# Kernel optimization log

Measured on AMD Instinct MI355X. Metric: run time of the kernel, lower is better.

## Reference

```python
import jax, jax.numpy as jnp
import numpy as np

EMBED_DIM = 768
NUM_HEADS = 12
HEAD_DIM = EMBED_DIM // NUM_HEADS
SCALING = HEAD_DIM ** -0.5


def setup_inputs() -> dict:
    key = jax.random.key(0)
    ks = jax.random.split(key, 12)
    B, S, E, H = 4, 1024, EMBED_DIM, NUM_HEADS
    inp = {
        "hidden_states": jax.random.normal(ks[0], (B, S, E), dtype=jnp.float32),
        "pos_row": jax.random.randint(ks[1], (B, S), 0, 64, dtype=jnp.int32),
        "pos_col": jax.random.randint(ks[2], (B, S), 0, 32, dtype=jnp.int32),
        "q_w": jax.random.normal(ks[3], (E, E), dtype=jnp.float32) * 0.02,
        "q_b": jnp.zeros((E,), dtype=jnp.float32),
        "k_w": jax.random.normal(ks[4], (E, E), dtype=jnp.float32) * 0.02,
        "k_b": jnp.zeros((E,), dtype=jnp.float32),
        "v_w": jax.random.normal(ks[5], (E, E), dtype=jnp.float32) * 0.02,
        "v_b": jnp.zeros((E,), dtype=jnp.float32),
        "o_w": jax.random.normal(ks[6], (E, E), dtype=jnp.float32) * 0.02,
        "o_b": jnp.zeros((E,), dtype=jnp.float32),
        "rel_table": jax.random.normal(ks[7], (4, H), dtype=jnp.float32) * 0.02,
    }
    return inp


def _generate_bias(pos_row, pos_col, rel_table):
    # relative row/col differences: [B, S, S]
    rel_row = pos_row[:, :, None] - pos_row[:, None, :]
    rel_col = pos_col[:, :, None] - pos_col[:, None, :]
    rel_cell = jnp.abs(rel_row) + jnp.abs(rel_col)
    # table index: other=0, same row=1, same col=2, same cell=3 (priority order as in torch code)
    idx = jnp.where(rel_row == 0, 1, 0)
    idx = jnp.where(rel_col == 0, 2, idx)
    idx = jnp.where(rel_cell == 0, 3, idx)
    # gather: [B, S, S, H] -> [B, H, S, S]
    bias = rel_table[idx]
    return jnp.transpose(bias, (0, 3, 1, 2))


def reference(hidden_states, pos_row, pos_col, q_w, q_b, k_w, k_b, v_w, v_b, o_w, o_b, rel_table):
    B, S, E = hidden_states.shape
    H, D = NUM_HEADS, HEAD_DIM

    def shape(x):  # [B, S, E] -> [B, H, S, D]
        return jnp.transpose(x.reshape(B, S, H, D), (0, 2, 1, 3))

    q = shape((hidden_states @ q_w.T + q_b) * SCALING)
    k = shape(hidden_states @ k_w.T + k_b)
    v = shape(hidden_states @ v_w.T + v_b)

    # [B, H, S, S]
    attn = jnp.einsum("bhqd,bhkd->bhqk", q, k)
    attn = attn + _generate_bias(pos_row, pos_col, rel_table)
    attn = jax.nn.softmax(attn, axis=-1)

    out = jnp.einsum("bhqk,bhkd->bhqd", attn, v)  # [B, H, S, D]
    out = jnp.transpose(out, (0, 2, 1, 3)).reshape(B, S, E)
    return out @ o_w.T + o_b
```

## Files before the change

kernel.cpp:

```cpp
#include <hip/hip_runtime.h>

#define NHEADS 12
#define HDIM   64
#define EMB    768
#define SEQ    1024
#define BATCH  4
#define MTOT   (BATCH * SEQ)

typedef __bf16 bf16x8 __attribute__((ext_vector_type(8)));
typedef float  f32x4  __attribute__((ext_vector_type(4)));

#define GLB(p) ((const __attribute__((address_space(1))) uint32_t*)(p))
#define LDS(p) ((__attribute__((address_space(3))) uint32_t*)(p))

__device__ __forceinline__ uint bfr(float f) {
    uint u = __float_as_uint(f);
    return (u + 0x7fffu + ((u >> 16) & 1u)) >> 16;
}

__global__ __launch_bounds__(256) void split_f32(
    const float* __restrict__ x, ushort* __restrict__ hi,
    ushort* __restrict__ lo, int n4)
{
    int i = blockIdx.x * 256 + threadIdx.x;
    if (i >= n4) return;
    float4 v = ((const float4*)x)[i];
    float f[4] = {v.x, v.y, v.z, v.w};
    ushort hh[4], ll[4];
#pragma unroll
    for (int j = 0; j < 4; ++j) {
        uint h = bfr(f[j]);
        float hf = __uint_as_float(h << 16);
        ll[j] = (ushort)bfr(f[j] - hf);
        hh[j] = (ushort)h;
    }
    ushort4 hv = {hh[0], hh[1], hh[2], hh[3]};
    ushort4 lv = {ll[0], ll[1], ll[2], ll[3]};
    ((ushort4*)hi)[i] = hv;
    ((ushort4*)lo)[i] = lv;
}

__global__ __launch_bounds__(256) void split_w4(
    const float* __restrict__ w0, const float* __restrict__ w1,
    const float* __restrict__ w2, const float* __restrict__ w3,
    ushort* __restrict__ wch, ushort* __restrict__ wcl,
    ushort* __restrict__ woh, ushort* __restrict__ wol, int n4)
{
    const int y = blockIdx.y;
    const float* src = (y == 0) ? w0 : (y == 1) ? w1 : (y == 2) ? w2 : w3;
    ushort* hi = (y < 3) ? (wch + (size_t)y * (EMB * EMB)) : woh;
    ushort* lo = (y < 3) ? (wcl + (size_t)y * (EMB * EMB)) : wol;
    int i = blockIdx.x * 256 + threadIdx.x;
    if (i >= n4) return;
    float4 v = ((const float4*)src)[i];
    float f[4] = {v.x, v.y, v.z, v.w};
    ushort hh[4], ll[4];
#pragma unroll
    for (int j = 0; j < 4; ++j) {
        uint h = bfr(f[j]);
        float hf = __uint_as_float(h << 16);
        ll[j] = (ushort)bfr(f[j] - hf);
        hh[j] = (ushort)h;
    }
    ushort4 hv = {hh[0], hh[1], hh[2], hh[3]};
    ushort4 lv = {ll[0], ll[1], ll[2], ll[3]};
    ((ushort4*)hi)[i] = hv;
    ((ushort4*)lo)[i] = lv;
}

template <int MODE, int BM>
__global__ __launch_bounds__(256) void gemm_mfma(
    const ushort* __restrict__ Ah, const ushort* __restrict__ Al,
    const ushort* __restrict__ Wh, const ushort* __restrict__ Wl,
    const float* __restrict__ b0, const float* __restrict__ b1,
    const float* __restrict__ b2,
    ushort* __restrict__ q16, ushort* __restrict__ k16,
    ushort* __restrict__ vT16, float* __restrict__ o0)
{
    constexpr int SA = BM * 64;
    constexpr int SB = 8192;
    constexpr int TS = 2 * SA + 2 * SB;
    constexpr int MFRAG = BM / 32;
    constexpr int WMS = BM / 2;

    __shared__ __align__(16) char ldsc[2 * TS];

    const int t  = threadIdx.x;
    const int w  = t >> 6;
    const int l  = t & 63;
    const int m0 = blockIdx.x * BM;
    const int n0 = blockIdx.y * 128;
    const int wm = w >> 1;
    const int wn = w & 1;

    const char* gb[4] = {
        (const char*)Ah + (size_t)m0 * 1536,
        (const char*)Al + (size_t)m0 * 1536,
        (const char*)Wh + (size_t)n0 * 1536,
        (const char*)Wl + (size_t)n0 * 1536};

    int aoff[MFRAG], boff[4];
#pragma unroll
    for (int i = 0; i < MFRAG; ++i) {
        int row = wm * WMS + i * 16 + (l & 15);
        aoff[i] = row * 64 + ((((l >> 4) ^ ((row >> 1) & 3))) << 4);
    }
#pragma unroll
    for (int i = 0; i < 4; ++i) {
        int rn = wn * 64 + i * 16 + (l & 15);
        boff[i] = rn * 64 + ((((l >> 4) ^ ((rn >> 1) & 3))) << 4);
    }

    auto stage = [&](int ks, int buf) {
        const size_t kb = (size_t)ks * 64;
        char* dst = ldsc + buf * TS;
#pragma unroll
        for (int tt = 0; tt < 4; ++tt) {
            const int tsz  = (tt < 2) ? SA : SB;
            const int tbas = (tt == 0) ? 0 : (tt == 1) ? SA : (tt == 2) ? 2 * SA : 2 * SA + SB;
#pragma unroll
            for (int p = 0; p < tsz; p += 4096) {
                const int soff = p + w * 1024 + l * 16;
                const int srow = soff >> 6;
                const int slot = (soff >> 4) & 3;
                const size_t go = (size_t)srow * 1536 +
                                  ((slot ^ ((srow >> 1) & 3)) << 4) + kb;
                __builtin_amdgcn_global_load_lds(GLB(gb[tt] + go),
                                                 LDS(dst + tbas + p + w * 1024), 16, 0, 0);
            }
        }
    };

    f32x4 acc[MFRAG][4] = {};

    stage(0, 0);
    __syncthreads();

    for (int ks = 0; ks < 24; ++ks) {
        if (ks + 1 < 24) stage(ks + 1, (ks + 1) & 1);

        const char* cur = ldsc + (ks & 1) * TS;
        bf16x8 ah[MFRAG], al[MFRAG], bh[4], bl[4];
#pragma unroll
        for (int i = 0; i < MFRAG; ++i) {
            ah[i] = *(const bf16x8*)(cur + aoff[i]);
            al[i] = *(const bf16x8*)(cur + SA + aoff[i]);
        }
#pragma unroll
        for (int i = 0; i < 4; ++i) {
            bh[i] = *(const bf16x8*)(cur + 2 * SA + boff[i]);
            bl[i] = *(const bf16x8*)(cur + 2 * SA + SB + boff[i]);
        }
#pragma unroll
        for (int i = 0; i < MFRAG; ++i)
#pragma unroll
            for (int j = 0; j < 4; ++j) {
                acc[i][j] = __builtin_amdgcn_mfma_f32_16x16x32_bf16(ah[i], bh[j], acc[i][j], 0, 0, 0);
                acc[i][j] = __builtin_amdgcn_mfma_f32_16x16x32_bf16(ah[i], bl[j], acc[i][j], 0, 0, 0);
                acc[i][j] = __builtin_amdgcn_mfma_f32_16x16x32_bf16(al[i], bh[j], acc[i][j], 0, 0, 0);
            }
        __syncthreads();
    }

    const int mrow_base = m0 + wm * WMS + ((l >> 4) << 2);

    if (MODE == 1) {
        const int which = (n0 >= 1536) ? 2 : (n0 >= 768 ? 1 : 0);
        const float* bp = (which == 0) ? b0 : (which == 1 ? b1 : b2);
        ushort* op = (which == 0) ? q16 : (which == 1 ? k16 : vT16);
        const float scale = (which == 0) ? 0.125f : 1.0f;
        const int nin_base = n0 - which * 768 + wn * 64 + (l & 15);
#pragma unroll
        for (int j = 0; j < 4; ++j) {
            const int n_in = nin_base + j * 16;
            const float bv = bp[n_in];
            const int h = n_in >> 6, d = n_in & 63;
#pragma unroll
            for (int i = 0; i < MFRAG; ++i)
#pragma unroll
                for (int r = 0; r < 4; ++r) {
                    const int m = mrow_base + i * 16 + r;
                    const int bb = m >> 10, s = m & 1023;
                    const ushort u = (ushort)bfr((acc[i][j][r] + bv) * scale);
                    const size_t dst = (which == 2)
                        ? ((size_t)((bb * NHEADS + h) * HDIM + d) * SEQ + s)
                        : ((size_t)((bb * NHEADS + h) * SEQ + s) * HDIM + d);
                    op[dst] = u;
                }
        }
    } else {
        const int nin_base = n0 + wn * 64 + (l & 15);
#pragma unroll
        for (int j = 0; j < 4; ++j) {
            const int n_in = nin_base + j * 16;
            const float bv = b0[n_in];
#pragma unroll
            for (int i = 0; i < MFRAG; ++i)
#pragma unroll
                for (int r = 0; r < 4; ++r) {
                    const int m = mrow_base + i * 16 + r;
                    o0[(size_t)m * 768 + n_in] = acc[i][j][r] + bv;
                }
        }
    }
}

#define QPOFF  0
#define KOFF   8192
#define VOFF   24576
#define POSOFF 40960

__global__ __launch_bounds__(256) void attn_mfma(
    const ushort* __restrict__ q16, const ushort* __restrict__ k16,
    const ushort* __restrict__ vT16, const int* __restrict__ pos_row,
    const int* __restrict__ pos_col, const float* __restrict__ rel_table,
    ushort* __restrict__ aoh, ushort* __restrict__ aol)
{
    __shared__ __align__(16) char lds[41472];

    const int t  = threadIdx.x;
    const int w  = t >> 6;
    const int l  = t & 63;
    const int bh = blockIdx.y;
    const int b  = bh / NHEADS;
    const int h  = bh - b * NHEADS;
    const int q0g = blockIdx.x * 64;

    const char* qb  = (const char*)(q16 + (size_t)bh * SEQ * HDIM);
    const char* kb  = (const char*)(k16 + (size_t)bh * SEQ * HDIM);
    const char* vtb = (const char*)(vT16 + (size_t)bh * HDIM * SEQ);

    const float t0 = rel_table[0 * NHEADS + h];
    const float t1 = rel_table[1 * NHEADS + h];
    const float t2 = rel_table[2 * NHEADS + h];
    const float t3 = rel_table[3 * NHEADS + h];

    const int o1 = t * 16, o2 = o1 + 4096;
    const int r1 = o1 >> 7, r2 = o2 >> 7;
    const int kq1 = o1 ^ ((r1 & 7) << 4);
    const int kq2 = o2 ^ ((r2 & 7) << 4);
    const int vs1 = r1 * 2048 + (((((o1 >> 4) & 7) ^ (r1 & 7))) << 4);
    const int vs2 = r2 * 2048 + (((((o2 >> 4) & 7) ^ (r2 & 7))) << 4);

    auto stage_kv = [&](int kt, int buf) {
        const int k0g = kt * 64;
        __builtin_amdgcn_global_load_lds(GLB(kb + (size_t)k0g * 128 + kq1),
                                         LDS(lds + KOFF + buf * 8192 + w * 1024), 16, 0, 0);
        __builtin_amdgcn_global_load_lds(GLB(kb + (size_t)k0g * 128 + kq2),
                                         LDS(lds + KOFF + buf * 8192 + w * 1024 + 4096), 16, 0, 0);
        __builtin_amdgcn_global_load_lds(GLB(vtb + (size_t)k0g * 2 + vs1),
                                         LDS(lds + VOFF + buf * 8192 + w * 1024), 16, 0, 0);
        __builtin_amdgcn_global_load_lds(GLB(vtb + (size_t)k0g * 2 + vs2),
                                         LDS(lds + VOFF + buf * 8192 + w * 1024 + 4096), 16, 0, 0);
        if (t < 64) {
            int pr = pos_row[b * SEQ + k0g + t];
            int pc = pos_col[b * SEQ + k0g + t];
            *(int*)(lds + POSOFF + buf * 256 + t * 4) = (pr << 8) | pc;
        }
    };

    __builtin_amdgcn_global_load_lds(GLB(qb + (size_t)q0g * 128 + kq1),
                                     LDS(lds + QPOFF + w * 1024), 16, 0, 0);
    __builtin_amdgcn_global_load_lds(GLB(qb + (size_t)q0g * 128 + kq2),
                                     LDS(lds + QPOFF + w * 1024 + 4096), 16, 0, 0);
    stage_kv(0, 0);

    const int qrow_g = q0g + w * 16 + (l & 15);
    const int pq = (pos_row[b * SEQ + qrow_g] << 8) | pos_col[b * SEQ + qrow_g];

    __syncthreads();

    bf16x8 qf[2];
    const int qrl = w * 16 + (l & 15);
#pragma unroll
    for (int ks = 0; ks < 2; ++ks)
        qf[ks] = *(const bf16x8*)(lds + QPOFF + qrl * 128 +
                                  ((((l >> 4) + 4 * ks) ^ (qrl & 7)) << 4));

    f32x4 pv[4] = {};
    float m_run = -1e30f, l_run = 0.0f;

    const int prow = l & 15;
    const int pswz = (prow & 7) << 4;
    const int pwbase = QPOFF + w * 2048 + prow * 128;

    for (int kt = 0; kt < 16; ++kt) {
        const int cb = kt & 1;
        if (kt + 1 < 16) stage_kv(kt + 1, cb ^ 1);
        const char* kbuf = lds + KOFF + cb * 8192;
        const char* vbuf = lds + VOFF + cb * 8192;
        const char* pbuf = lds + POSOFF + cb * 256;

        f32x4 sacc[4] = {};
#pragma unroll
        for (int ks = 0; ks < 2; ++ks) {
            const bf16x8 qq = qf[ks];
#pragma unroll
            for (int j = 0; j < 4; ++j) {
                const int krow = j * 16 + (l & 15);
                const bf16x8 kf = *(const bf16x8*)(kbuf + krow * 128 +
                                                   ((((l >> 4) + 4 * ks) ^ (krow & 7)) << 4));
                sacc[j] = __builtin_amdgcn_mfma_f32_16x16x32_bf16(kf, qq, sacc[j], 0, 0, 0);
            }
        }

        int4 pk4[4];
#pragma unroll
        for (int j = 0; j < 4; ++j)
            pk4[j] = *(const int4*)(pbuf + (l >> 4) * 16 + j * 64);

        float sv[16];
#pragma unroll
        for (int j = 0; j < 4; ++j) {
            const int pkk[4] = {pk4[j].x, pk4[j].y, pk4[j].z, pk4[j].w};
#pragma unroll
            for (int r = 0; r < 4; ++r) {
                const int dd = pq ^ pkk[r];
                const float bs = ((dd & 0xFF00) == 0)
                                     ? (((dd & 0xFF) == 0) ? t3 : t1)
                                     : (((dd & 0xFF) == 0) ? t2 : t0);
                sv[j * 4 + r] = sacc[j][r] + bs;
            }
        }
        float pm = sv[0];
#pragma unroll
        for (int i = 1; i < 16; ++i) pm = fmaxf(pm, sv[i]);
        pm = fmaxf(pm, __shfl_xor(pm, 16));
        pm = fmaxf(pm, __shfl_xor(pm, 32));
        const float mnew = fmaxf(m_run, pm);
        float psum = 0.0f;
#pragma unroll
        for (int i = 0; i < 16; ++i) {
            sv[i] = __expf(sv[i] - mnew);
            psum += sv[i];
        }
        psum += __shfl_xor(psum, 16);
        psum += __shfl_xor(psum, 32);
        const float alpha = __expf(m_run - mnew);
        l_run = l_run * alpha + psum;
        m_run = mnew;

#pragma unroll
        for (int r = 0; r < 4; ++r) {
            const float ar = __shfl(alpha, (l >> 4) * 4 + r);
#pragma unroll
            for (int i = 0; i < 4; ++i) pv[i][r] *= ar;
        }

#pragma unroll
        for (int j = 0; j < 4; ++j)
#pragma unroll
            for (int p2 = 0; p2 < 2; ++p2) {
                const uint u = bfr(sv[j * 4 + 2 * p2]) | (bfr(sv[j * 4 + 2 * p2 + 1]) << 16);
                const int adr = pwbase + (((l >> 4) * 8 + 4 * p2 + 32 * j) ^ pswz);
                *(uint*)(lds + adr) = u;
            }

#pragma unroll
        for (int ks = 0; ks < 2; ++ks) {
            const bf16x8 pf = *(const bf16x8*)(lds + pwbase +
                                               ((((l >> 4) + 4 * ks) << 4) ^ pswz));
#pragma unroll
            for (int i = 0; i < 4; ++i) {
                const int vrow = i * 16 + (l & 15);
                const bf16x8 vf = *(const bf16x8*)(vbuf + vrow * 128 +
                                                   ((((l >> 4) + 4 * ks) ^ (vrow & 7)) << 4));
                pv[i] = __builtin_amdgcn_mfma_f32_16x16x32_bf16(pf, vf, pv[i], 0, 0, 0);
            }
        }
        __syncthreads();
    }

    const float rinv = 1.0f / l_run;
#pragma unroll
    for (int r = 0; r < 4; ++r) {
        const float inv = __shfl(rinv, (l >> 4) * 4 + r);
        const int mrow = b * SEQ + q0g + w * 16 + (l >> 4) * 4 + r;
        const size_t base = (size_t)mrow * 768 + h * 64 + prow;
#pragma unroll
        for (int i = 0; i < 4; ++i) {
            const float o = pv[i][r] * inv;
            const uint hu = bfr(o);
            const float hf = __uint_as_float(hu << 16);
            const uint lu = bfr(o - hf);
            aoh[base + 16 * i] = (ushort)hu;
            aol[base + 16 * i] = (ushort)lu;
        }
    }
}

extern "C" void kernel_launch(void* const* d_in, const int* in_sizes, int n_in,
                              void* d_out, int out_size, void* d_ws, size_t ws_size,
                              hipStream_t stream)
{
    const float* hs      = (const float*)d_in[0];
    const int*   pos_row = (const int*)d_in[1];
    const int*   pos_col = (const int*)d_in[2];
    const float* q_w     = (const float*)d_in[3];
    const float* q_b     = (const float*)d_in[4];
    const float* k_w     = (const float*)d_in[5];
    const float* k_b     = (const float*)d_in[6];
    const float* v_w     = (const float*)d_in[7];
    const float* v_b     = (const float*)d_in[8];
    const float* o_w     = (const float*)d_in[9];
    const float* o_b     = (const float*)d_in[10];
    const float* rel_tab = (const float*)d_in[11];

    char* ws = (char*)d_ws;
    const size_t HS_N = (size_t)MTOT * EMB;
    const size_t W_N  = (size_t)EMB * EMB;
    ushort* hsh = (ushort*)ws;  ws += HS_N * 2;
    ushort* hsl = (ushort*)ws;  ws += HS_N * 2;
    ushort* wch = (ushort*)ws;  ws += 3 * W_N * 2;
    ushort* wcl = (ushort*)ws;  ws += 3 * W_N * 2;
    ushort* woh = (ushort*)ws;  ws += W_N * 2;
    ushort* wol = (ushort*)ws;  ws += W_N * 2;
    ushort* aoh = (ushort*)ws;  ws += HS_N * 2;
    ushort* aol = (ushort*)ws;  ws += HS_N * 2;
    ushort* q16 = (ushort*)ws;  ws += HS_N * 2;
    ushort* k16 = (ushort*)ws;  ws += HS_N * 2;
    ushort* vT16 = (ushort*)ws; ws += HS_N * 2;

    split_f32<<<(int)(HS_N / 4 / 256), 256, 0, stream>>>(hs, hsh, hsl, (int)(HS_N / 4));
    split_w4<<<dim3((int)(W_N / 4 / 256), 4), 256, 0, stream>>>(
        q_w, k_w, v_w, o_w, wch, wcl, woh, wol, (int)(W_N / 4));

    gemm_mfma<1, 128><<<dim3(MTOT / 128, 2304 / 128), 256, 0, stream>>>(
        hsh, hsl, wch, wcl, q_b, k_b, v_b, q16, k16, vT16, nullptr);

    attn_mfma<<<dim3(SEQ / 64, BATCH * NHEADS), 256, 0, stream>>>(
        q16, k16, vT16, pos_row, pos_col, rel_tab, aoh, aol);

    gemm_mfma<0, 64><<<dim3(MTOT / 64, EMB / 128), 256, 0, stream>>>(
        aoh, aol, woh, wol, o_b, nullptr, nullptr,
        nullptr, nullptr, nullptr, (float*)d_out);
}
```

Measured before the change: 229.7 us.

## Merge split kernels, use 512-thread GEMM blocks, vectorize V-transpose stores

Fuses the two fp32-to-bf16 hi/lo split kernels into one launch with a flat block index. Doubles GEMM blocks to 8 waves arranged 2x4, each wave covering a 32-column slice, and rewrites staging so each thread issues one 16-byte LDS load per 8 KB chunk. The V projection epilogue now writes four consecutive sequence elements as one ushort4 store into the transposed layout instead of four scalar stores. These aim to cut launch overhead, raise wave-level parallelism per tile, and reduce scattered stores, at the cost of halving per-wave MFMA work relative to LDS fragment reads.

```diff
diff --git a/kernel.cpp b/kernel.cpp
--- a/kernel.cpp
+++ b/kernel.cpp
@@ -18,13 +18,30 @@
     return (u + 0x7fffu + ((u >> 16) & 1u)) >> 16;
 }
 
-__global__ __launch_bounds__(256) void split_f32(
-    const float* __restrict__ x, ushort* __restrict__ hi,
-    ushort* __restrict__ lo, int n4)
+__global__ __launch_bounds__(256) void split_all(
+    const float* __restrict__ hs,
+    const float* __restrict__ w0, const float* __restrict__ w1,
+    const float* __restrict__ w2, const float* __restrict__ w3,
+    ushort* __restrict__ hsh, ushort* __restrict__ hsl,
+    ushort* __restrict__ wch, ushort* __restrict__ wcl,
+    ushort* __restrict__ woh, ushort* __restrict__ wol)
 {
-    int i = blockIdx.x * 256 + threadIdx.x;
-    if (i >= n4) return;
-    float4 v = ((const float4*)x)[i];
+    const int bx = blockIdx.x;
+    const float* src;
+    ushort *hi, *lo;
+    int i;
+    if (bx < 3072) {
+        src = hs; hi = hsh; lo = hsl;
+        i = bx * 256 + threadIdx.x;
+    } else {
+        const int y = (bx - 3072) / 576;
+        const int r = (bx - 3072) - y * 576;
+        src = (y == 0) ? w0 : (y == 1) ? w1 : (y == 2) ? w2 : w3;
+        hi = (y < 3) ? (wch + (size_t)y * (EMB * EMB)) : woh;
+        lo = (y < 3) ? (wcl + (size_t)y * (EMB * EMB)) : wol;
+        i = r * 256 + threadIdx.x;
+    }
+    float4 v = ((const float4*)src)[i];
     float f[4] = {v.x, v.y, v.z, v.w};
     ushort hh[4], ll[4];
 #pragma unroll
@@ -40,36 +57,8 @@
     ((ushort4*)lo)[i] = lv;
 }
 
-__global__ __launch_bounds__(256) void split_w4(
-    const float* __restrict__ w0, const float* __restrict__ w1,
-    const float* __restrict__ w2, const float* __restrict__ w3,
-    ushort* __restrict__ wch, ushort* __restrict__ wcl,
-    ushort* __restrict__ woh, ushort* __restrict__ wol, int n4)
-{
-    const int y = blockIdx.y;
-    const float* src = (y == 0) ? w0 : (y == 1) ? w1 : (y == 2) ? w2 : w3;
-    ushort* hi = (y < 3) ? (wch + (size_t)y * (EMB * EMB)) : woh;
-    ushort* lo = (y < 3) ? (wcl + (size_t)y * (EMB * EMB)) : wol;
-    int i = blockIdx.x * 256 + threadIdx.x;
-    if (i >= n4) return;
-    float4 v = ((const float4*)src)[i];
-    float f[4] = {v.x, v.y, v.z, v.w};
-    ushort hh[4], ll[4];
-#pragma unroll
-    for (int j = 0; j < 4; ++j) {
-        uint h = bfr(f[j]);
-        float hf = __uint_as_float(h << 16);
-        ll[j] = (ushort)bfr(f[j] - hf);
-        hh[j] = (ushort)h;
-    }
-    ushort4 hv = {hh[0], hh[1], hh[2], hh[3]};
-    ushort4 lv = {ll[0], ll[1], ll[2], ll[3]};
-    ((ushort4*)hi)[i] = hv;
-    ((ushort4*)lo)[i] = lv;
-}
-
 template <int MODE, int BM>
-__global__ __launch_bounds__(256) void gemm_mfma(
+__global__ __launch_bounds__(512) void gemm_mfma(
     const ushort* __restrict__ Ah, const ushort* __restrict__ Al,
     const ushort* __restrict__ Wh, const ushort* __restrict__ Wl,
     const float* __restrict__ b0, const float* __restrict__ b1,
@@ -90,8 +79,8 @@
     const int l  = t & 63;
     const int m0 = blockIdx.x * BM;
     const int n0 = blockIdx.y * 128;
-    const int wm = w >> 1;
-    const int wn = w & 1;
+    const int wm = w >> 2;
+    const int wn = w & 3;
 
     const char* gb[4] = {
         (const char*)Ah + (size_t)m0 * 1536,
@@ -99,15 +88,15 @@
         (const char*)Wh + (size_t)n0 * 1536,
         (const char*)Wl + (size_t)n0 * 1536};
 
-    int aoff[MFRAG], boff[4];
+    int aoff[MFRAG], boff[2];
 #pragma unroll
     for (int i = 0; i < MFRAG; ++i) {
         int row = wm * WMS + i * 16 + (l & 15);
         aoff[i] = row * 64 + ((((l >> 4) ^ ((row >> 1) & 3))) << 4);
     }
 #pragma unroll
-    for (int i = 0; i < 4; ++i) {
-        int rn = wn * 64 + i * 16 + (l & 15);
+    for (int i = 0; i < 2; ++i) {
+        int rn = wn * 32 + i * 16 + (l & 15);
         boff[i] = rn * 64 + ((((l >> 4) ^ ((rn >> 1) & 3))) << 4);
     }
 
@@ -117,21 +106,24 @@
 #pragma unroll
         for (int tt = 0; tt < 4; ++tt) {
             const int tsz  = (tt < 2) ? SA : SB;
-            const int tbas = (tt == 0) ? 0 : (tt == 1) ? SA : (tt == 2) ? 2 * SA : 2 * SA + SB;
-#pragma unroll
-            for (int p = 0; p < tsz; p += 4096) {
-                const int soff = p + w * 1024 + l * 16;
-                const int srow = soff >> 6;
-                const int slot = (soff >> 4) & 3;
-                const size_t go = (size_t)srow * 1536 +
-                                  ((slot ^ ((srow >> 1) & 3)) << 4) + kb;
-                __builtin_amdgcn_global_load_lds(GLB(gb[tt] + go),
-                                                 LDS(dst + tbas + p + w * 1024), 16, 0, 0);
+            const int tbas = (tt == 0) ? 0 : (tt == 1) ? SA
+                           : (tt == 2) ? 2 * SA : 2 * SA + SB;
+#pragma unroll
+            for (int p = 0; p < tsz; p += 8192) {
+                const int soff = p + t * 16;
+                if (soff < tsz) {
+                    const int srow = soff >> 6;
+                    const int slot = (soff >> 4) & 3;
+                    const size_t go = (size_t)srow * 1536 +
+                                      ((slot ^ ((srow >> 1) & 3)) << 4) + kb;
+                    __builtin_amdgcn_global_load_lds(GLB(gb[tt] + go),
+                                                     LDS(dst + tbas + soff), 16, 0, 0);
+                }
             }
         }
     };
 
-    f32x4 acc[MFRAG][4] = {};
+    f32x4 acc[MFRAG][2] = {};
 
     stage(0, 0);
     __syncthreads();
@@ -140,21 +132,21 @@
         if (ks + 1 < 24) stage(ks + 1, (ks + 1) & 1);
 
         const char* cur = ldsc + (ks & 1) * TS;
-        bf16x8 ah[MFRAG], al[MFRAG], bh[4], bl[4];
+        bf16x8 ah[MFRAG], al[MFRAG], bh[2], bl[2];
 #pragma unroll
         for (int i = 0; i < MFRAG; ++i) {
             ah[i] = *(const bf16x8*)(cur + aoff[i]);
             al[i] = *(const bf16x8*)(cur + SA + aoff[i]);
         }
 #pragma unroll
-        for (int i = 0; i < 4; ++i) {
+        for (int i = 0; i < 2; ++i) {
             bh[i] = *(const bf16x8*)(cur + 2 * SA + boff[i]);
             bl[i] = *(const bf16x8*)(cur + 2 * SA + SB + boff[i]);
         }
 #pragma unroll
         for (int i = 0; i < MFRAG; ++i)
 #pragma unroll
-            for (int j = 0; j < 4; ++j) {
+            for (int j = 0; j < 2; ++j) {
                 acc[i][j] = __builtin_amdgcn_mfma_f32_16x16x32_bf16(ah[i], bh[j], acc[i][j], 0, 0, 0);
                 acc[i][j] = __builtin_amdgcn_mfma_f32_16x16x32_bf16(ah[i], bl[j], acc[i][j], 0, 0, 0);
                 acc[i][j] = __builtin_amdgcn_mfma_f32_16x16x32_bf16(al[i], bh[j], acc[i][j], 0, 0, 0);
@@ -167,31 +159,47 @@
     if (MODE == 1) {
         const int which = (n0 >= 1536) ? 2 : (n0 >= 768 ? 1 : 0);
         const float* bp = (which == 0) ? b0 : (which == 1 ? b1 : b2);
-        ushort* op = (which == 0) ? q16 : (which == 1 ? k16 : vT16);
         const float scale = (which == 0) ? 0.125f : 1.0f;
-        const int nin_base = n0 - which * 768 + wn * 64 + (l & 15);
-#pragma unroll
-        for (int j = 0; j < 4; ++j) {
-            const int n_in = nin_base + j * 16;
-            const float bv = bp[n_in];
-            const int h = n_in >> 6, d = n_in & 63;
-#pragma unroll
-            for (int i = 0; i < MFRAG; ++i)
-#pragma unroll
-                for (int r = 0; r < 4; ++r) {
-                    const int m = mrow_base + i * 16 + r;
+        const int nin_base = n0 - which * 768 + wn * 32 + (l & 15);
+        if (which == 2) {
+#pragma unroll
+            for (int j = 0; j < 2; ++j) {
+                const int n_in = nin_base + j * 16;
+                const float bv = b2[n_in];
+                const int h = n_in >> 6, d = n_in & 63;
+#pragma unroll
+                for (int i = 0; i < MFRAG; ++i) {
+                    const int m = mrow_base + i * 16;
                     const int bb = m >> 10, s = m & 1023;
-                    const ushort u = (ushort)bfr((acc[i][j][r] + bv) * scale);
-                    const size_t dst = (which == 2)
-                        ? ((size_t)((bb * NHEADS + h) * HDIM + d) * SEQ + s)
-                        : ((size_t)((bb * NHEADS + h) * SEQ + s) * HDIM + d);
-                    op[dst] = u;
+                    ushort4 pk = {(ushort)bfr(acc[i][j][0] + bv),
+                                  (ushort)bfr(acc[i][j][1] + bv),
+                                  (ushort)bfr(acc[i][j][2] + bv),
+                                  (ushort)bfr(acc[i][j][3] + bv)};
+                    *(ushort4*)(vT16 + (size_t)((bb * NHEADS + h) * HDIM + d) * SEQ + s) = pk;
                 }
+            }
+        } else {
+            ushort* op = (which == 0) ? q16 : k16;
+#pragma unroll
+            for (int j = 0; j < 2; ++j) {
+                const int n_in = nin_base + j * 16;
+                const float bv = bp[n_in];
+                const int h = n_in >> 6, d = n_in & 63;
+#pragma unroll
+                for (int i = 0; i < MFRAG; ++i)
+#pragma unroll
+                    for (int r = 0; r < 4; ++r) {
+                        const int m = mrow_base + i * 16 + r;
+                        const int bb = m >> 10, s = m & 1023;
+                        op[(size_t)((bb * NHEADS + h) * SEQ + s) * HDIM + d] =
+                            (ushort)bfr((acc[i][j][r] + bv) * scale);
+                    }
+            }
         }
     } else {
-        const int nin_base = n0 + wn * 64 + (l & 15);
-#pragma unroll
-        for (int j = 0; j < 4; ++j) {
+        const int nin_base = n0 + wn * 32 + (l & 15);
+#pragma unroll
+        for (int j = 0; j < 2; ++j) {
             const int n_in = nin_base + j * 16;
             const float bv = b0[n_in];
 #pragma unroll
@@ -421,17 +429,16 @@
     ushort* k16 = (ushort*)ws;  ws += HS_N * 2;
     ushort* vT16 = (ushort*)ws; ws += HS_N * 2;
 
-    split_f32<<<(int)(HS_N / 4 / 256), 256, 0, stream>>>(hs, hsh, hsl, (int)(HS_N / 4));
-    split_w4<<<dim3((int)(W_N / 4 / 256), 4), 256, 0, stream>>>(
-        q_w, k_w, v_w, o_w, wch, wcl, woh, wol, (int)(W_N / 4));
-
-    gemm_mfma<1, 128><<<dim3(MTOT / 128, 2304 / 128), 256, 0, stream>>>(
+    split_all<<<3072 + 4 * 576, 256, 0, stream>>>(
+        hs, q_w, k_w, v_w, o_w, hsh, hsl, wch, wcl, woh, wol);
+
+    gemm_mfma<1, 128><<<dim3(MTOT / 128, 2304 / 128), 512, 0, stream>>>(
         hsh, hsl, wch, wcl, q_b, k_b, v_b, q16, k16, vT16, nullptr);
 
     attn_mfma<<<dim3(SEQ / 64, BATCH * NHEADS), 256, 0, stream>>>(
         q16, k16, vT16, pos_row, pos_col, rel_tab, aoh, aol);
 
-    gemm_mfma<0, 64><<<dim3(MTOT / 64, EMB / 128), 256, 0, stream>>>(
+    gemm_mfma<0, 64><<<dim3(MTOT / 64, EMB / 128), 512, 0, stream>>>(
         aoh, aol, woh, wol, o_b, nullptr, nullptr,
         nullptr, nullptr, nullptr, (float*)d_out);
 }
```

Result: faster. 209.1 us (-9.0%).
